# Kernel optimization log

Measured on AMD Instinct MI355X. Metric: run time of the kernel, lower is better.

The kernel has to match this reference:

```python
import jax, jax.numpy as jnp
import numpy as np

N_NODES = 50000
N_EDGES = 800000
D = 128
N_GRAPHS = 64


def setup_inputs() -> dict:
    key = jax.random.key(0)
    ks = jax.random.split(key, 9)
    x = jax.random.normal(ks[0], (N_NODES, D), dtype=jnp.float32)
    edge_index = jax.random.randint(ks[1], (2, N_EDGES), 0, N_NODES, dtype=jnp.int32)
    batch = jnp.sort(jax.random.randint(ks[2], (N_NODES,), 0, N_GRAPHS, dtype=jnp.int32))
    s = 1.0 / np.sqrt(D)
    W1 = jax.random.normal(ks[3], (D, D), jnp.float32) * s
    W2 = jax.random.normal(ks[4], (D, D), jnp.float32) * s
    W3 = jax.random.normal(ks[5], (D, D), jnp.float32) * s
    b1 = jnp.zeros((D,), jnp.float32)
    b2 = jnp.zeros((D,), jnp.float32)
    b3 = jnp.zeros((D,), jnp.float32)
    return {"x": x, "W1": W1, "b1": b1, "W2": W2, "b2": b2, "W3": W3, "b3": b3,
            "edge_index": edge_index, "batch": batch}


def _gcn_conv(x, W, b, src, dst, deg_inv_sqrt):
    # PyG GCNConv: x' = D^{-1/2} (A+I) D^{-1/2} (x W) + b
    h = x @ W                                    # [N, D]
    norm = (deg_inv_sqrt[src] * deg_inv_sqrt[dst])[:, None]   # [E, 1]
    agg = jax.ops.segment_sum(h[src] * norm, dst, num_segments=N_NODES)
    # self-loop contribution: norm_ii = deg_i^{-1}
    agg = agg + (deg_inv_sqrt * deg_inv_sqrt)[:, None] * h
    return agg + b


def reference(x, W1, b1, W2, b2, W3, b3, edge_index, batch):
    src, dst = edge_index[0], edge_index[1]
    # degree on A + I (self-loops added), edge weight 1
    deg = jax.ops.segment_sum(jnp.ones((N_EDGES,), x.dtype), dst,
                              num_segments=N_NODES) + 1.0
    deg_inv_sqrt = jax.lax.rsqrt(deg)
    h = jax.nn.relu(_gcn_conv(x, W1, b1, src, dst, deg_inv_sqrt))
    h = jax.nn.relu(_gcn_conv(h, W2, b2, src, dst, deg_inv_sqrt))
    h = _gcn_conv(h, W3, b3, src, dst, deg_inv_sqrt)
    # global_max_pool over graph ids
    return jax.ops.segment_max(h, batch, num_segments=N_GRAPHS)
```

## Files before the change

### kernel.cpp

```cpp
#include <hip/hip_runtime.h>
#include <float.h>
#include <math.h>

#define D 128
#define PCHUNK 64
#define NBUCK 256
#define BROWS 196
#define BCAP 4096
#define ACHUNK 3125

typedef _Float16 half8 __attribute__((ext_vector_type(8)));
typedef _Float16 half2v __attribute__((ext_vector_type(2)));
typedef float f32x4 __attribute__((ext_vector_type(4)));

__device__ __forceinline__ unsigned encf(float x) {
    unsigned u = __float_as_uint(x);
    return (u & 0x80000000u) ? ~u : (u | 0x80000000u);
}
__device__ __forceinline__ float decf(unsigned e) {
    unsigned u = (e & 0x80000000u) ? (e & 0x7FFFFFFFu) : ~e;
    return __uint_as_float(u);
}

__global__ __launch_bounds__(256) void binA_kernel(const int* __restrict__ src,
                                                   const int* __restrict__ dst,
                                                   int* __restrict__ gcnt,
                                                   uint2* __restrict__ gpair, int ne) {
    __shared__ int lh[NBUCK], ssc[NBUCK], lstart[NBUCK], gbase[NBUCK], loff[NBUCK];
    __shared__ uint2 stage[ACHUNK + 8];
    int t = threadIdx.x;
    int e0 = blockIdx.x * ACHUNK;
    int e1 = min(e0 + ACHUNK, ne);
    lh[t] = 0;
    __syncthreads();
    for (int e = e0 + t; e < e1; e += 256) atomicAdd(&lh[dst[e] / BROWS], 1);
    __syncthreads();
    ssc[t] = lh[t];
    __syncthreads();
    for (int off = 1; off < NBUCK; off <<= 1) {
        int u = (t >= off) ? ssc[t - off] : 0;
        __syncthreads();
        ssc[t] += u;
        __syncthreads();
    }
    int st = ssc[t] - lh[t];
    lstart[t] = st;
    loff[t] = st;
    if (lh[t] > 0) gbase[t] = atomicAdd(&gcnt[t], lh[t]);
    __syncthreads();
    for (int e = e0 + t; e < e1; e += 256) {
        int s = src[e], d = dst[e];
        int pos = atomicAdd(&loff[d / BROWS], 1);
        stage[pos] = make_uint2((unsigned)s, (unsigned)d);
    }
    __syncthreads();
    int m = e1 - e0;
    for (int i = t; i < m; i += 256) {
        uint2 pr = stage[i];
        int b = (int)pr.y / BROWS;
        int gpos = b * BCAP + gbase[b] + (i - lstart[b]);
        if (gpos < (b + 1) * BCAP) gpair[gpos] = pr;
    }
}

__global__ __launch_bounds__(256) void scanB_kernel(const int* __restrict__ gcnt,
                                                    int* __restrict__ bstart,
                                                    unsigned* __restrict__ outEnc, int nout) {
    __shared__ int s[NBUCK], c[NBUCK];
    int t = threadIdx.x;
    for (int j = t; j < nout; j += 256) outEnc[j] = 0x007FFFFFu;
    c[t] = gcnt[t];
    s[t] = c[t];
    __syncthreads();
    for (int off = 1; off < NBUCK; off <<= 1) {
        int u = (t >= off) ? s[t - off] : 0;
        __syncthreads();
        s[t] += u;
        __syncthreads();
    }
    bstart[t] = s[t] - c[t];
    if (t == NBUCK - 1) bstart[NBUCK] = s[NBUCK - 1];
}

__global__ __launch_bounds__(256) void binB_kernel(const uint2* __restrict__ gpair,
                                                   const int* __restrict__ gcnt,
                                                   const int* __restrict__ bstart,
                                                   int* __restrict__ rowptr,
                                                   float* __restrict__ disv,
                                                   int* __restrict__ csr, int n) {
    __shared__ int lh[256], ssc[256], lstart[256], loff[256];
    __shared__ int cstage[BCAP];
    int b = blockIdx.x, t = threadIdx.x;
    int m = min(gcnt[b], BCAP);
    int row0 = b * BROWS;
    int nrows = min(BROWS, n - row0);
    if (nrows <= 0) return;
    const uint2* mp = gpair + (size_t)b * BCAP;
    lh[t] = 0;
    __syncthreads();
    for (int i = t; i < m; i += 256) atomicAdd(&lh[(int)mp[i].y - row0], 1);
    __syncthreads();
    ssc[t] = lh[t];
    __syncthreads();
    for (int off = 1; off < 256; off <<= 1) {
        int u = (t >= off) ? ssc[t - off] : 0;
        __syncthreads();
        ssc[t] += u;
        __syncthreads();
    }
    int st = ssc[t] - lh[t];
    lstart[t] = st;
    loff[t] = st;
    __syncthreads();
    int bs = bstart[b];
    if (t <= nrows) rowptr[row0 + t] = bs + lstart[t];
    if (t < nrows) disv[row0 + t] = rsqrtf((float)lh[t] + 1.0f);
    for (int i = t; i < m; i += 256) {
        uint2 pr = mp[i];
        int pos = atomicAdd(&loff[(int)pr.y - row0], 1);
        cstage[pos] = (int)pr.x;
    }
    __syncthreads();
    for (int i = t; i < m; i += 256) csr[bs + i] = cstage[i];
}

__global__ void pack3_kernel(const float* __restrict__ W1, const float* __restrict__ W2,
                             const float* __restrict__ W3, _Float16* __restrict__ Wp1,
                             _Float16* __restrict__ Wp2, _Float16* __restrict__ Wp3) {
    int gi = blockIdx.x * blockDim.x + threadIdx.x;
    int w = gi >> 14, i = gi & 16383;
    const float* W = (w == 0) ? W1 : (w == 1) ? W2 : W3;
    _Float16* Wp = (w == 0) ? Wp1 : (w == 1) ? Wp2 : Wp3;
    int j = i & 7, l = (i >> 3) & 63, t = (i >> 9) & 7, s = (i >> 12) & 3;
    int k = s * 32 + ((l >> 4) << 3) + j;
    int c = t * 16 + (l & 15);
    Wp[i] = (_Float16)W[k * 128 + c];
}

template <bool F32SRC>
__global__ __launch_bounds__(256) void gemm_mfma(const void* __restrict__ Xsrc,
                                                 const _Float16* __restrict__ Wp,
                                                 const float* __restrict__ disv,
                                                 _Float16* __restrict__ Gh,
                                                 int ntiles, int n) {
    __shared__ _Float16 Wl[16384];
    int tid = threadIdx.x;
    {
        const uint4* s4 = (const uint4*)Wp;
        uint4* d4 = (uint4*)Wl;
#pragma unroll
        for (int i = 0; i < 8; i++) d4[tid + 256 * i] = s4[tid + 256 * i];
    }
    __syncthreads();
    int wave = tid >> 6, lane = tid & 63;
    int m = lane & 15, quad = lane >> 4;
    const half8* wfrag = (const half8*)Wl;
    const _Float16* Xh = (const _Float16*)Xsrc;
    const float* Xf = (const float*)Xsrc;

    for (int tile0 = blockIdx.x * 4; tile0 < ntiles; tile0 += gridDim.x * 4) {
        int tile = tile0 + wave;
        if (tile >= ntiles) break;
        int arow = tile * 16 + m;
        if (arow >= n) arow = n - 1;

        f32x4 acc[8];
#pragma unroll
        for (int t = 0; t < 8; t++) acc[t] = (f32x4){0.f, 0.f, 0.f, 0.f};

#pragma unroll
        for (int s = 0; s < 4; s++) {
            half8 a;
            if (F32SRC) {
                float4 lo = *(const float4*)(Xf + (size_t)arow * D + s * 32 + quad * 8);
                float4 hi = *(const float4*)(Xf + (size_t)arow * D + s * 32 + quad * 8 + 4);
                a[0] = (_Float16)lo.x; a[1] = (_Float16)lo.y; a[2] = (_Float16)lo.z; a[3] = (_Float16)lo.w;
                a[4] = (_Float16)hi.x; a[5] = (_Float16)hi.y; a[6] = (_Float16)hi.z; a[7] = (_Float16)hi.w;
            } else {
                a = *(const half8*)(Xh + (size_t)arow * D + s * 32 + quad * 8);
            }
#pragma unroll
            for (int t = 0; t < 8; t++) {
                half8 b = wfrag[(s * 8 + t) * 64 + lane];
                acc[t] = __builtin_amdgcn_mfma_f32_16x16x32_f16(a, b, acc[t], 0, 0, 0);
            }
        }
        int orow0 = tile * 16 + quad * 4;
        if (orow0 + 3 < n) {
            float d0 = disv[orow0], d1 = disv[orow0 + 1], d2 = disv[orow0 + 2], d3 = disv[orow0 + 3];
#pragma unroll
            for (int t = 0; t < 8; t++) {
                int col = t * 16 + m;
                Gh[(size_t)(orow0 + 0) * D + col] = (_Float16)(acc[t][0] * d0);
                Gh[(size_t)(orow0 + 1) * D + col] = (_Float16)(acc[t][1] * d1);
                Gh[(size_t)(orow0 + 2) * D + col] = (_Float16)(acc[t][2] * d2);
                Gh[(size_t)(orow0 + 3) * D + col] = (_Float16)(acc[t][3] * d3);
            }
        } else {
#pragma unroll
            for (int t = 0; t < 8; t++) {
                int col = t * 16 + m;
#pragma unroll
                for (int r = 0; r < 4; r++) {
                    int orow = orow0 + r;
                    if (orow < n) Gh[(size_t)orow * D + col] = (_Float16)(acc[t][r] * disv[orow]);
                }
            }
        }
    }
}

__global__ __launch_bounds__(256) void agg_f16(const _Float16* __restrict__ G,
                                               const int* __restrict__ rowptr,
                                               const int* __restrict__ csr,
                                               const float* __restrict__ disv,
                                               const float* __restrict__ bias,
                                               _Float16* __restrict__ Out, int n, int relu) {
    int wave = threadIdx.x >> 6, lane = threadIdx.x & 63;
    int node = blockIdx.x * 4 + wave;
    if (node >= n) return;
    const half2v* G2 = (const half2v*)G;
    half2v sv = G2[(size_t)node * 64 + lane];
    float ax = (float)sv[0], ay = (float)sv[1];
    int e = rowptr[node], end = rowptr[node + 1];
    for (; e + 8 <= end; e += 8) {
        int s0 = csr[e], s1 = csr[e + 1], s2 = csr[e + 2], s3 = csr[e + 3];
        int s4 = csr[e + 4], s5 = csr[e + 5], s6 = csr[e + 6], s7 = csr[e + 7];
        half2v v0 = G2[(size_t)s0 * 64 + lane];
        half2v v1 = G2[(size_t)s1 * 64 + lane];
        half2v v2 = G2[(size_t)s2 * 64 + lane];
        half2v v3 = G2[(size_t)s3 * 64 + lane];
        half2v v4 = G2[(size_t)s4 * 64 + lane];
        half2v v5 = G2[(size_t)s5 * 64 + lane];
        half2v v6 = G2[(size_t)s6 * 64 + lane];
        half2v v7 = G2[(size_t)s7 * 64 + lane];
        ax += (((float)v0[0] + (float)v1[0]) + ((float)v2[0] + (float)v3[0])) +
              (((float)v4[0] + (float)v5[0]) + ((float)v6[0] + (float)v7[0]));
        ay += (((float)v0[1] + (float)v1[1]) + ((float)v2[1] + (float)v3[1])) +
              (((float)v4[1] + (float)v5[1]) + ((float)v6[1] + (float)v7[1]));
    }
    for (; e + 4 <= end; e += 4) {
        int s0 = csr[e], s1 = csr[e + 1], s2 = csr[e + 2], s3 = csr[e + 3];
        half2v v0 = G2[(size_t)s0 * 64 + lane];
        half2v v1 = G2[(size_t)s1 * 64 + lane];
        half2v v2 = G2[(size_t)s2 * 64 + lane];
        half2v v3 = G2[(size_t)s3 * 64 + lane];
        ax += ((float)v0[0] + (float)v1[0]) + ((float)v2[0] + (float)v3[0]);
        ay += ((float)v0[1] + (float)v1[1]) + ((float)v2[1] + (float)v3[1]);
    }
    for (; e < end; e++) {
        half2v v = G2[(size_t)csr[e] * 64 + lane];
        ax += (float)v[0]; ay += (float)v[1];
    }
    float dd = disv[node];
    int c = lane * 2;
    float ox = fmaf(dd, ax, bias[c]);
    float oy = fmaf(dd, ay, bias[c + 1]);
    if (relu) { ox = fmaxf(ox, 0.f); oy = fmaxf(oy, 0.f); }
    half2v o;
    o[0] = (_Float16)ox; o[1] = (_Float16)oy;
    ((half2v*)Out)[(size_t)node * 64 + lane] = o;
}

__global__ __launch_bounds__(128) void pool_kernel(const _Float16* __restrict__ H,
                                                   const int* __restrict__ batch,
                                                   unsigned* __restrict__ outEnc, int n) {
    int d = threadIdx.x;
    int start = blockIdx.x * PCHUNK;
    if (start >= n) return;
    int end = min(start + PCHUNK, n);
    int curg = batch[start];
    float cur = -INFINITY;
    for (int i = start; i < end; i++) {
        float v = (float)H[(size_t)i * D + d];
        int g = batch[i];
        if (g != curg) { atomicMax(&outEnc[curg * D + d], encf(cur)); cur = v; curg = g; }
        else cur = fmaxf(cur, v);
    }
    atomicMax(&outEnc[curg * D + d], encf(cur));
}

__global__ void decode_kernel(const unsigned* __restrict__ outEnc, float* __restrict__ out, int n) {
    int i = blockIdx.x * blockDim.x + threadIdx.x;
    if (i < n) out[i] = decf(outEnc[i]);
}

extern "C" void kernel_launch(void* const* d_in, const int* in_sizes, int n_in,
                              void* d_out, int out_size, void* d_ws, size_t ws_size,
                              hipStream_t stream) {
    const float* x  = (const float*)d_in[0];
    const float* W1 = (const float*)d_in[1];
    const float* b1 = (const float*)d_in[2];
    const float* W2 = (const float*)d_in[3];
    const float* b2 = (const float*)d_in[4];
    const float* W3 = (const float*)d_in[5];
    const float* b3 = (const float*)d_in[6];
    const int* ei    = (const int*)d_in[7];
    const int* batch = (const int*)d_in[8];

    int n  = in_sizes[0] / D;
    int ne = in_sizes[7] / 2;
    const int* src = ei;
    const int* dst = ei + ne;

    char* p = (char*)d_ws;
    auto alloc = [&](size_t bytes) -> void* {
        void* q = (void*)p;
        p += (bytes + 255) & ~(size_t)255;
        return q;
    };
    _Float16* Gh  = (_Float16*)alloc((size_t)n * D * 2);
    _Float16* Hh  = (_Float16*)alloc((size_t)n * D * 2);
    _Float16* Wp1 = (_Float16*)alloc((size_t)D * D * 2);
    _Float16* Wp2 = (_Float16*)alloc((size_t)D * D * 2);
    _Float16* Wp3 = (_Float16*)alloc((size_t)D * D * 2);
    int* gcnt     = (int*)alloc((size_t)NBUCK * 4);
    int* bstart   = (int*)alloc((size_t)(NBUCK + 1) * 4);
    uint2* gpair  = (uint2*)alloc((size_t)NBUCK * BCAP * 8);
    int* rowptr   = (int*)alloc((size_t)(n + 1) * 4);
    int* csr      = (int*)alloc((size_t)ne * 4);
    float* disv   = (float*)alloc((size_t)n * 4);
    unsigned* outEnc = (unsigned*)alloc((size_t)out_size * 4);

    hipMemsetAsync(gcnt, 0, (size_t)NBUCK * 4, stream);

    int nblocksA = (ne + ACHUNK - 1) / ACHUNK;
    binA_kernel<<<nblocksA, 256, 0, stream>>>(src, dst, gcnt, gpair, ne);
    scanB_kernel<<<1, 256, 0, stream>>>(gcnt, bstart, outEnc, out_size);
    binB_kernel<<<NBUCK, 256, 0, stream>>>(gpair, gcnt, bstart, rowptr, disv, csr, n);
    pack3_kernel<<<192, 256, 0, stream>>>(W1, W2, W3, Wp1, Wp2, Wp3);

    int ntiles = (n + 15) / 16;
    int gemm_blocks = 512;
    int agg_blocks  = (n + 3) / 4;

    gemm_mfma<true><<<gemm_blocks, 256, 0, stream>>>(x, Wp1, disv, Gh, ntiles, n);
    agg_f16<<<agg_blocks, 256, 0, stream>>>(Gh, rowptr, csr, disv, b1, Hh, n, 1);
    gemm_mfma<false><<<gemm_blocks, 256, 0, stream>>>(Hh, Wp2, disv, Gh, ntiles, n);
    agg_f16<<<agg_blocks, 256, 0, stream>>>(Gh, rowptr, csr, disv, b2, Hh, n, 1);
    gemm_mfma<false><<<gemm_blocks, 256, 0, stream>>>(Hh, Wp3, disv, Gh, ntiles, n);
    agg_f16<<<agg_blocks, 256, 0, stream>>>(Gh, rowptr, csr, disv, b3, Hh, n, 0);

    pool_kernel<<<(n + PCHUNK - 1) / PCHUNK, 128, 0, stream>>>(Hh, batch, outEnc, n);
    decode_kernel<<<(out_size + 255) / 256, 256, 0, stream>>>(outEnc, (float*)d_out, out_size);
}
```

Before: 265.4 us.

## Fuse aggregation with next-layer GEMM and final aggregation with max-pool

```diff
diff --git a/kernel.cpp b/kernel.cpp
--- a/kernel.cpp
+++ b/kernel.cpp
@@ -3,7 +3,6 @@
 #include <math.h>
 
 #define D 128
-#define PCHUNK 64
 #define NBUCK 256
 #define BROWS 196
 #define BCAP 4096
@@ -22,206 +21,12 @@
     return __uint_as_float(u);
 }
 
-__global__ __launch_bounds__(256) void binA_kernel(const int* __restrict__ src,
-                                                   const int* __restrict__ dst,
-                                                   int* __restrict__ gcnt,
-                                                   uint2* __restrict__ gpair, int ne) {
-    __shared__ int lh[NBUCK], ssc[NBUCK], lstart[NBUCK], gbase[NBUCK], loff[NBUCK];
-    __shared__ uint2 stage[ACHUNK + 8];
-    int t = threadIdx.x;
-    int e0 = blockIdx.x * ACHUNK;
-    int e1 = min(e0 + ACHUNK, ne);
-    lh[t] = 0;
-    __syncthreads();
-    for (int e = e0 + t; e < e1; e += 256) atomicAdd(&lh[dst[e] / BROWS], 1);
-    __syncthreads();
-    ssc[t] = lh[t];
-    __syncthreads();
-    for (int off = 1; off < NBUCK; off <<= 1) {
-        int u = (t >= off) ? ssc[t - off] : 0;
-        __syncthreads();
-        ssc[t] += u;
-        __syncthreads();
-    }
-    int st = ssc[t] - lh[t];
-    lstart[t] = st;
-    loff[t] = st;
-    if (lh[t] > 0) gbase[t] = atomicAdd(&gcnt[t], lh[t]);
-    __syncthreads();
-    for (int e = e0 + t; e < e1; e += 256) {
-        int s = src[e], d = dst[e];
-        int pos = atomicAdd(&loff[d / BROWS], 1);
-        stage[pos] = make_uint2((unsigned)s, (unsigned)d);
-    }
-    __syncthreads();
-    int m = e1 - e0;
-    for (int i = t; i < m; i += 256) {
-        uint2 pr = stage[i];
-        int b = (int)pr.y / BROWS;
-        int gpos = b * BCAP + gbase[b] + (i - lstart[b]);
-        if (gpos < (b + 1) * BCAP) gpair[gpos] = pr;
-    }
-}
-
-__global__ __launch_bounds__(256) void scanB_kernel(const int* __restrict__ gcnt,
-                                                    int* __restrict__ bstart,
-                                                    unsigned* __restrict__ outEnc, int nout) {
-    __shared__ int s[NBUCK], c[NBUCK];
-    int t = threadIdx.x;
-    for (int j = t; j < nout; j += 256) outEnc[j] = 0x007FFFFFu;
-    c[t] = gcnt[t];
-    s[t] = c[t];
-    __syncthreads();
-    for (int off = 1; off < NBUCK; off <<= 1) {
-        int u = (t >= off) ? s[t - off] : 0;
-        __syncthreads();
-        s[t] += u;
-        __syncthreads();
-    }
-    bstart[t] = s[t] - c[t];
-    if (t == NBUCK - 1) bstart[NBUCK] = s[NBUCK - 1];
-}
-
-__global__ __launch_bounds__(256) void binB_kernel(const uint2* __restrict__ gpair,
-                                                   const int* __restrict__ gcnt,
-                                                   const int* __restrict__ bstart,
-                                                   int* __restrict__ rowptr,
-                                                   float* __restrict__ disv,
-                                                   int* __restrict__ csr, int n) {
-    __shared__ int lh[256], ssc[256], lstart[256], loff[256];
-    __shared__ int cstage[BCAP];
-    int b = blockIdx.x, t = threadIdx.x;
-    int m = min(gcnt[b], BCAP);
-    int row0 = b * BROWS;
-    int nrows = min(BROWS, n - row0);
-    if (nrows <= 0) return;
-    const uint2* mp = gpair + (size_t)b * BCAP;
-    lh[t] = 0;
-    __syncthreads();
-    for (int i = t; i < m; i += 256) atomicAdd(&lh[(int)mp[i].y - row0], 1);
-    __syncthreads();
-    ssc[t] = lh[t];
-    __syncthreads();
-    for (int off = 1; off < 256; off <<= 1) {
-        int u = (t >= off) ? ssc[t - off] : 0;
-        __syncthreads();
-        ssc[t] += u;
-        __syncthreads();
-    }
-    int st = ssc[t] - lh[t];
-    lstart[t] = st;
-    loff[t] = st;
-    __syncthreads();
-    int bs = bstart[b];
-    if (t <= nrows) rowptr[row0 + t] = bs + lstart[t];
-    if (t < nrows) disv[row0 + t] = rsqrtf((float)lh[t] + 1.0f);
-    for (int i = t; i < m; i += 256) {
-        uint2 pr = mp[i];
-        int pos = atomicAdd(&loff[(int)pr.y - row0], 1);
-        cstage[pos] = (int)pr.x;
-    }
-    __syncthreads();
-    for (int i = t; i < m; i += 256) csr[bs + i] = cstage[i];
-}
-
-__global__ void pack3_kernel(const float* __restrict__ W1, const float* __restrict__ W2,
-                             const float* __restrict__ W3, _Float16* __restrict__ Wp1,
-                             _Float16* __restrict__ Wp2, _Float16* __restrict__ Wp3) {
-    int gi = blockIdx.x * blockDim.x + threadIdx.x;
-    int w = gi >> 14, i = gi & 16383;
-    const float* W = (w == 0) ? W1 : (w == 1) ? W2 : W3;
-    _Float16* Wp = (w == 0) ? Wp1 : (w == 1) ? Wp2 : Wp3;
-    int j = i & 7, l = (i >> 3) & 63, t = (i >> 9) & 7, s = (i >> 12) & 3;
-    int k = s * 32 + ((l >> 4) << 3) + j;
-    int c = t * 16 + (l & 15);
-    Wp[i] = (_Float16)W[k * 128 + c];
-}
-
-template <bool F32SRC>
-__global__ __launch_bounds__(256) void gemm_mfma(const void* __restrict__ Xsrc,
-                                                 const _Float16* __restrict__ Wp,
-                                                 const float* __restrict__ disv,
-                                                 _Float16* __restrict__ Gh,
-                                                 int ntiles, int n) {
-    __shared__ _Float16 Wl[16384];
-    int tid = threadIdx.x;
-    {
-        const uint4* s4 = (const uint4*)Wp;
-        uint4* d4 = (uint4*)Wl;
-#pragma unroll
-        for (int i = 0; i < 8; i++) d4[tid + 256 * i] = s4[tid + 256 * i];
-    }
-    __syncthreads();
-    int wave = tid >> 6, lane = tid & 63;
-    int m = lane & 15, quad = lane >> 4;
-    const half8* wfrag = (const half8*)Wl;
-    const _Float16* Xh = (const _Float16*)Xsrc;
-    const float* Xf = (const float*)Xsrc;
-
-    for (int tile0 = blockIdx.x * 4; tile0 < ntiles; tile0 += gridDim.x * 4) {
-        int tile = tile0 + wave;
-        if (tile >= ntiles) break;
-        int arow = tile * 16 + m;
-        if (arow >= n) arow = n - 1;
-
-        f32x4 acc[8];
-#pragma unroll
-        for (int t = 0; t < 8; t++) acc[t] = (f32x4){0.f, 0.f, 0.f, 0.f};
-
-#pragma unroll
-        for (int s = 0; s < 4; s++) {
-            half8 a;
-            if (F32SRC) {
-                float4 lo = *(const float4*)(Xf + (size_t)arow * D + s * 32 + quad * 8);
-                float4 hi = *(const float4*)(Xf + (size_t)arow * D + s * 32 + quad * 8 + 4);
-                a[0] = (_Float16)lo.x; a[1] = (_Float16)lo.y; a[2] = (_Float16)lo.z; a[3] = (_Float16)lo.w;
-                a[4] = (_Float16)hi.x; a[5] = (_Float16)hi.y; a[6] = (_Float16)hi.z; a[7] = (_Float16)hi.w;
-            } else {
-                a = *(const half8*)(Xh + (size_t)arow * D + s * 32 + quad * 8);
-            }
-#pragma unroll
-            for (int t = 0; t < 8; t++) {
-                half8 b = wfrag[(s * 8 + t) * 64 + lane];
-                acc[t] = __builtin_amdgcn_mfma_f32_16x16x32_f16(a, b, acc[t], 0, 0, 0);
-            }
-        }
-        int orow0 = tile * 16 + quad * 4;
-        if (orow0 + 3 < n) {
-            float d0 = disv[orow0], d1 = disv[orow0 + 1], d2 = disv[orow0 + 2], d3 = disv[orow0 + 3];
-#pragma unroll
-            for (int t = 0; t < 8; t++) {
-                int col = t * 16 + m;
-                Gh[(size_t)(orow0 + 0) * D + col] = (_Float16)(acc[t][0] * d0);
-                Gh[(size_t)(orow0 + 1) * D + col] = (_Float16)(acc[t][1] * d1);
-                Gh[(size_t)(orow0 + 2) * D + col] = (_Float16)(acc[t][2] * d2);
-                Gh[(size_t)(orow0 + 3) * D + col] = (_Float16)(acc[t][3] * d3);
-            }
-        } else {
-#pragma unroll
-            for (int t = 0; t < 8; t++) {
-                int col = t * 16 + m;
-#pragma unroll
-                for (int r = 0; r < 4; r++) {
-                    int orow = orow0 + r;
-                    if (orow < n) Gh[(size_t)orow * D + col] = (_Float16)(acc[t][r] * disv[orow]);
-                }
-            }
-        }
-    }
-}
-
-__global__ __launch_bounds__(256) void agg_f16(const _Float16* __restrict__ G,
-                                               const int* __restrict__ rowptr,
-                                               const int* __restrict__ csr,
-                                               const float* __restrict__ disv,
-                                               const float* __restrict__ bias,
-                                               _Float16* __restrict__ Out, int n, int relu) {
-    int wave = threadIdx.x >> 6, lane = threadIdx.x & 63;
-    int node = blockIdx.x * 4 + wave;
-    if (node >= n) return;
-    const half2v* G2 = (const half2v*)G;
+__device__ __forceinline__ void gather_row(const half2v* __restrict__ G2,
+                                           const int* __restrict__ rowptr,
+                                           const int* __restrict__ csr,
+                                           int node, int lane, float& ax, float& ay) {
     half2v sv = G2[(size_t)node * 64 + lane];
-    float ax = (float)sv[0], ay = (float)sv[1];
+    ax = (float)sv[0]; ay = (float)sv[1];
     int e = rowptr[node], end = rowptr[node + 1];
     for (; e + 8 <= end; e += 8) {
         int s0 = csr[e], s1 = csr[e + 1], s2 = csr[e + 2], s3 = csr[e + 3];
@@ -252,32 +57,302 @@
         half2v v = G2[(size_t)csr[e] * 64 + lane];
         ax += (float)v[0]; ay += (float)v[1];
     }
-    float dd = disv[node];
-    int c = lane * 2;
-    float ox = fmaf(dd, ax, bias[c]);
-    float oy = fmaf(dd, ay, bias[c + 1]);
-    if (relu) { ox = fmaxf(ox, 0.f); oy = fmaxf(oy, 0.f); }
-    half2v o;
-    o[0] = (_Float16)ox; o[1] = (_Float16)oy;
-    ((half2v*)Out)[(size_t)node * 64 + lane] = o;
-}
-
-__global__ __launch_bounds__(128) void pool_kernel(const _Float16* __restrict__ H,
-                                                   const int* __restrict__ batch,
-                                                   unsigned* __restrict__ outEnc, int n) {
-    int d = threadIdx.x;
-    int start = blockIdx.x * PCHUNK;
-    if (start >= n) return;
-    int end = min(start + PCHUNK, n);
-    int curg = batch[start];
-    float cur = -INFINITY;
-    for (int i = start; i < end; i++) {
-        float v = (float)H[(size_t)i * D + d];
-        int g = batch[i];
-        if (g != curg) { atomicMax(&outEnc[curg * D + d], encf(cur)); cur = v; curg = g; }
-        else cur = fmaxf(cur, v);
-    }
-    atomicMax(&outEnc[curg * D + d], encf(cur));
+}
+
+__global__ __launch_bounds__(256) void binA_kernel(const int* __restrict__ src,
+                                                   const int* __restrict__ dst,
+                                                   int* __restrict__ gcnt,
+                                                   uint2* __restrict__ gpair, int ne) {
+    __shared__ int lh[NBUCK], ssc[NBUCK], lstart[NBUCK], gbase[NBUCK], loff[NBUCK];
+    __shared__ uint2 stage[ACHUNK + 8];
+    int t = threadIdx.x;
+    int e0 = blockIdx.x * ACHUNK;
+    int e1 = min(e0 + ACHUNK, ne);
+    lh[t] = 0;
+    __syncthreads();
+    for (int e = e0 + t; e < e1; e += 256) atomicAdd(&lh[dst[e] / BROWS], 1);
+    __syncthreads();
+    ssc[t] = lh[t];
+    __syncthreads();
+    for (int off = 1; off < NBUCK; off <<= 1) {
+        int u = (t >= off) ? ssc[t - off] : 0;
+        __syncthreads();
+        ssc[t] += u;
+        __syncthreads();
+    }
+    int st = ssc[t] - lh[t];
+    lstart[t] = st;
+    loff[t] = st;
+    if (lh[t] > 0) gbase[t] = atomicAdd(&gcnt[t], lh[t]);
+    __syncthreads();
+    for (int e = e0 + t; e < e1; e += 256) {
+        int s = src[e], d = dst[e];
+        int pos = atomicAdd(&loff[d / BROWS], 1);
+        stage[pos] = make_uint2((unsigned)s, (unsigned)d);
+    }
+    __syncthreads();
+    int m = e1 - e0;
+    for (int i = t; i < m; i += 256) {
+        uint2 pr = stage[i];
+        int b = (int)pr.y / BROWS;
+        int gpos = b * BCAP + gbase[b] + (i - lstart[b]);
+        if (gpos < (b + 1) * BCAP) gpair[gpos] = pr;
+    }
+}
+
+__global__ __launch_bounds__(256) void scanB_kernel(const int* __restrict__ gcnt,
+                                                    int* __restrict__ bstart,
+                                                    unsigned* __restrict__ outEnc, int nout) {
+    __shared__ int s[NBUCK], c[NBUCK];
+    int t = threadIdx.x;
+    for (int j = t; j < nout; j += 256) outEnc[j] = 0x007FFFFFu;
+    c[t] = gcnt[t];
+    s[t] = c[t];
+    __syncthreads();
+    for (int off = 1; off < NBUCK; off <<= 1) {
+        int u = (t >= off) ? s[t - off] : 0;
+        __syncthreads();
+        s[t] += u;
+        __syncthreads();
+    }
+    bstart[t] = s[t] - c[t];
+    if (t == NBUCK - 1) bstart[NBUCK] = s[NBUCK - 1];
+}
+
+__global__ __launch_bounds__(256) void binB_kernel(const uint2* __restrict__ gpair,
+                                                   const int* __restrict__ gcnt,
+                                                   const int* __restrict__ bstart,
+                                                   int* __restrict__ rowptr,
+                                                   float* __restrict__ disv,
+                                                   int* __restrict__ csr, int n) {
+    __shared__ int lh[256], ssc[256], lstart[256], loff[256];
+    __shared__ int cstage[BCAP];
+    int b = blockIdx.x, t = threadIdx.x;
+    int m = min(gcnt[b], BCAP);
+    int row0 = b * BROWS;
+    int nrows = min(BROWS, n - row0);
+    if (nrows <= 0) return;
+    const uint2* mp = gpair + (size_t)b * BCAP;
+    lh[t] = 0;
+    __syncthreads();
+    for (int i = t; i < m; i += 256) atomicAdd(&lh[(int)mp[i].y - row0], 1);
+    __syncthreads();
+    ssc[t] = lh[t];
+    __syncthreads();
+    for (int off = 1; off < 256; off <<= 1) {
+        int u = (t >= off) ? ssc[t - off] : 0;
+        __syncthreads();
+        ssc[t] += u;
+        __syncthreads();
+    }
+    int st = ssc[t] - lh[t];
+    lstart[t] = st;
+    loff[t] = st;
+    __syncthreads();
+    int bs = bstart[b];
+    if (t <= nrows) rowptr[row0 + t] = bs + lstart[t];
+    if (t < nrows) disv[row0 + t] = rsqrtf((float)lh[t] + 1.0f);
+    for (int i = t; i < m; i += 256) {
+        uint2 pr = mp[i];
+        int pos = atomicAdd(&loff[(int)pr.y - row0], 1);
+        cstage[pos] = (int)pr.x;
+    }
+    __syncthreads();
+    for (int i = t; i < m; i += 256) csr[bs + i] = cstage[i];
+}
+
+__global__ void pack3_kernel(const float* __restrict__ W1, const float* __restrict__ W2,
+                             const float* __restrict__ W3, _Float16* __restrict__ Wp1,
+                             _Float16* __restrict__ Wp2, _Float16* __restrict__ Wp3) {
+    int gi = blockIdx.x * blockDim.x + threadIdx.x;
+    int w = gi >> 14, i = gi & 16383;
+    const float* W = (w == 0) ? W1 : (w == 1) ? W2 : W3;
+    _Float16* Wp = (w == 0) ? Wp1 : (w == 1) ? Wp2 : Wp3;
+    int j = i & 7, l = (i >> 3) & 63, t = (i >> 9) & 7, s = (i >> 12) & 3;
+    int k = s * 32 + ((l >> 4) << 3) + j;
+    int c = t * 16 + (l & 15);
+    Wp[i] = (_Float16)W[k * 128 + c];
+}
+
+__global__ __launch_bounds__(256) void gemm_mfma(const float* __restrict__ Xf,
+                                                 const _Float16* __restrict__ Wp,
+                                                 const float* __restrict__ disv,
+                                                 _Float16* __restrict__ Gh,
+                                                 int ntiles, int n) {
+    __shared__ _Float16 Wl[16384];
+    int tid = threadIdx.x;
+    {
+        const uint4* s4 = (const uint4*)Wp;
+        uint4* d4 = (uint4*)Wl;
+#pragma unroll
+        for (int i = 0; i < 8; i++) d4[tid + 256 * i] = s4[tid + 256 * i];
+    }
+    __syncthreads();
+    int wave = tid >> 6, lane = tid & 63;
+    int m = lane & 15, quad = lane >> 4;
+    const half8* wfrag = (const half8*)Wl;
+
+    for (int tile0 = blockIdx.x * 4; tile0 < ntiles; tile0 += gridDim.x * 4) {
+        int tile = tile0 + wave;
+        if (tile >= ntiles) break;
+        int arow = tile * 16 + m;
+        if (arow >= n) arow = n - 1;
+
+        f32x4 acc[8];
+#pragma unroll
+        for (int t = 0; t < 8; t++) acc[t] = (f32x4){0.f, 0.f, 0.f, 0.f};
+
+#pragma unroll
+        for (int s = 0; s < 4; s++) {
+            half8 a;
+            float4 lo = *(const float4*)(Xf + (size_t)arow * D + s * 32 + quad * 8);
+            float4 hi = *(const float4*)(Xf + (size_t)arow * D + s * 32 + quad * 8 + 4);
+            a[0] = (_Float16)lo.x; a[1] = (_Float16)lo.y; a[2] = (_Float16)lo.z; a[3] = (_Float16)lo.w;
+            a[4] = (_Float16)hi.x; a[5] = (_Float16)hi.y; a[6] = (_Float16)hi.z; a[7] = (_Float16)hi.w;
+#pragma unroll
+            for (int t = 0; t < 8; t++) {
+                half8 b = wfrag[(s * 8 + t) * 64 + lane];
+                acc[t] = __builtin_amdgcn_mfma_f32_16x16x32_f16(a, b, acc[t], 0, 0, 0);
+            }
+        }
+        int orow0 = tile * 16 + quad * 4;
+        if (orow0 + 3 < n) {
+            float d0 = disv[orow0], d1 = disv[orow0 + 1], d2 = disv[orow0 + 2], d3 = disv[orow0 + 3];
+#pragma unroll
+            for (int t = 0; t < 8; t++) {
+                int col = t * 16 + m;
+                Gh[(size_t)(orow0 + 0) * D + col] = (_Float16)(acc[t][0] * d0);
+                Gh[(size_t)(orow0 + 1) * D + col] = (_Float16)(acc[t][1] * d1);
+                Gh[(size_t)(orow0 + 2) * D + col] = (_Float16)(acc[t][2] * d2);
+                Gh[(size_t)(orow0 + 3) * D + col] = (_Float16)(acc[t][3] * d3);
+            }
+        } else {
+#pragma unroll
+            for (int t = 0; t < 8; t++) {
+                int col = t * 16 + m;
+#pragma unroll
+                for (int r = 0; r < 4; r++) {
+                    int orow = orow0 + r;
+                    if (orow < n) Gh[(size_t)orow * D + col] = (_Float16)(acc[t][r] * disv[orow]);
+                }
+            }
+        }
+    }
+}
+
+__global__ __launch_bounds__(256) void fused_ag(const _Float16* __restrict__ Gin,
+                                                const _Float16* __restrict__ Wp,
+                                                const int* __restrict__ rowptr,
+                                                const int* __restrict__ csr,
+                                                const float* __restrict__ disv,
+                                                const float* __restrict__ bias,
+                                                _Float16* __restrict__ Gout,
+                                                int ntiles, int n) {
+    __shared__ _Float16 Wl[16384];
+    __shared__ __align__(16) _Float16 stage[4][2048];
+    int tid = threadIdx.x;
+    {
+        const uint4* s4 = (const uint4*)Wp;
+        uint4* d4 = (uint4*)Wl;
+#pragma unroll
+        for (int i = 0; i < 8; i++) d4[tid + 256 * i] = s4[tid + 256 * i];
+    }
+    __syncthreads();
+    int wave = tid >> 6, lane = tid & 63;
+    int tile = blockIdx.x * 4 + wave;
+    if (tile >= ntiles) return;
+    _Float16* st = stage[wave];
+    const half2v* G2 = (const half2v*)Gin;
+    int sqp = lane >> 2;
+    int j0 = (lane & 3) * 2;
+    float bx = bias[lane * 2], by = bias[lane * 2 + 1];
+
+    for (int p = 0; p < 16; p++) {
+        int node = tile * 16 + p;
+        float ox = 0.f, oy = 0.f;
+        if (node < n) {
+            float ax, ay;
+            gather_row(G2, rowptr, csr, node, lane, ax, ay);
+            float dd = disv[node];
+            ox = fmaxf(fmaf(dd, ax, bx), 0.f);
+            oy = fmaxf(fmaf(dd, ay, by), 0.f);
+        }
+        half2v o;
+        o[0] = (_Float16)ox; o[1] = (_Float16)oy;
+        *(half2v*)&st[sqp * 128 + (((p + sqp) & 15) << 3) + j0] = o;
+    }
+
+    int m = lane & 15, quad = lane >> 4;
+    const half8* wfrag = (const half8*)Wl;
+    f32x4 acc[8];
+#pragma unroll
+    for (int t = 0; t < 8; t++) acc[t] = (f32x4){0.f, 0.f, 0.f, 0.f};
+#pragma unroll
+    for (int s = 0; s < 4; s++) {
+        int sqc = s * 4 + quad;
+        half8 a = *(const half8*)&st[sqc * 128 + (((m + sqc) & 15) << 3)];
+#pragma unroll
+        for (int t = 0; t < 8; t++) {
+            half8 b = wfrag[(s * 8 + t) * 64 + lane];
+            acc[t] = __builtin_amdgcn_mfma_f32_16x16x32_f16(a, b, acc[t], 0, 0, 0);
+        }
+    }
+    int orow0 = tile * 16 + quad * 4;
+    if (orow0 + 3 < n) {
+        float d0 = disv[orow0], d1 = disv[orow0 + 1], d2 = disv[orow0 + 2], d3 = disv[orow0 + 3];
+#pragma unroll
+        for (int t = 0; t < 8; t++) {
+            int col = t * 16 + m;
+            Gout[(size_t)(orow0 + 0) * D + col] = (_Float16)(acc[t][0] * d0);
+            Gout[(size_t)(orow0 + 1) * D + col] = (_Float16)(acc[t][1] * d1);
+            Gout[(size_t)(orow0 + 2) * D + col] = (_Float16)(acc[t][2] * d2);
+            Gout[(size_t)(orow0 + 3) * D + col] = (_Float16)(acc[t][3] * d3);
+        }
+    } else {
+#pragma unroll
+        for (int t = 0; t < 8; t++) {
+            int col = t * 16 + m;
+#pragma unroll
+            for (int r = 0; r < 4; r++) {
+                int orow = orow0 + r;
+                if (orow < n) Gout[(size_t)orow * D + col] = (_Float16)(acc[t][r] * disv[orow]);
+            }
+        }
+    }
+}
+
+__global__ __launch_bounds__(256) void aggpool(const _Float16* __restrict__ Gin,
+                                               const int* __restrict__ rowptr,
+                                               const int* __restrict__ csr,
+                                               const float* __restrict__ disv,
+                                               const float* __restrict__ bias,
+                                               const int* __restrict__ batch,
+                                               unsigned* __restrict__ outEnc, int n) {
+    int wave = threadIdx.x >> 6, lane = threadIdx.x & 63;
+    int base = (blockIdx.x * 4 + wave) * 32;
+    if (base >= n) return;
+    int end = min(base + 32, n);
+    const half2v* G2 = (const half2v*)Gin;
+    float bx = bias[lane * 2], by = bias[lane * 2 + 1];
+    float mx = -INFINITY, my = -INFINITY;
+    int curg = batch[base];
+    for (int node = base; node < end; node++) {
+        float ax, ay;
+        gather_row(G2, rowptr, csr, node, lane, ax, ay);
+        float dd = disv[node];
+        float ox = fmaf(dd, ax, bx);
+        float oy = fmaf(dd, ay, by);
+        int g = batch[node];
+        if (g != curg) {
+            atomicMax(&outEnc[curg * D + lane * 2], encf(mx));
+            atomicMax(&outEnc[curg * D + lane * 2 + 1], encf(my));
+            mx = ox; my = oy; curg = g;
+        } else {
+            mx = fmaxf(mx, ox); my = fmaxf(my, oy);
+        }
+    }
+    atomicMax(&outEnc[curg * D + lane * 2], encf(mx));
+    atomicMax(&outEnc[curg * D + lane * 2 + 1], encf(my));
 }
 
 __global__ void decode_kernel(const unsigned* __restrict__ outEnc, float* __restrict__ out, int n) {
@@ -309,8 +384,8 @@
         p += (bytes + 255) & ~(size_t)255;
         return q;
     };
-    _Float16* Gh  = (_Float16*)alloc((size_t)n * D * 2);
-    _Float16* Hh  = (_Float16*)alloc((size_t)n * D * 2);
+    _Float16* GhA = (_Float16*)alloc((size_t)n * D * 2);
+    _Float16* GhB = (_Float16*)alloc((size_t)n * D * 2);
     _Float16* Wp1 = (_Float16*)alloc((size_t)D * D * 2);
     _Float16* Wp2 = (_Float16*)alloc((size_t)D * D * 2);
     _Float16* Wp3 = (_Float16*)alloc((size_t)D * D * 2);
@@ -331,16 +406,11 @@
     pack3_kernel<<<192, 256, 0, stream>>>(W1, W2, W3, Wp1, Wp2, Wp3);
 
     int ntiles = (n + 15) / 16;
-    int gemm_blocks = 512;
-    int agg_blocks  = (n + 3) / 4;
-
-    gemm_mfma<true><<<gemm_blocks, 256, 0, stream>>>(x, Wp1, disv, Gh, ntiles, n);
-    agg_f16<<<agg_blocks, 256, 0, stream>>>(Gh, rowptr, csr, disv, b1, Hh, n, 1);
-    gemm_mfma<false><<<gemm_blocks, 256, 0, stream>>>(Hh, Wp2, disv, Gh, ntiles, n);
-    agg_f16<<<agg_blocks, 256, 0, stream>>>(Gh, rowptr, csr, disv, b2, Hh, n, 1);
-    gemm_mfma<false><<<gemm_blocks, 256, 0, stream>>>(Hh, Wp3, disv, Gh, ntiles, n);
-    agg_f16<<<agg_blocks, 256, 0, stream>>>(Gh, rowptr, csr, disv, b3, Hh, n, 0);
-
-    pool_kernel<<<(n + PCHUNK - 1) / PCHUNK, 128, 0, stream>>>(Hh, batch, outEnc, n);
+    int fused_blocks = (ntiles + 3) / 4;
+
+    gemm_mfma<<<512, 256, 0, stream>>>(x, Wp1, disv, GhA, ntiles, n);
+    fused_ag<<<fused_blocks, 256, 0, stream>>>(GhA, Wp2, rowptr, csr, disv, b1, GhB, ntiles, n);
+    fused_ag<<<fused_blocks, 256, 0, stream>>>(GhB, Wp3, rowptr, csr, disv, b2, GhA, ntiles, n);
+    aggpool<<<(n + 127) / 128, 256, 0, stream>>>(GhA, rowptr, csr, disv, b3, batch, outEnc, n);
     decode_kernel<<<(out_size + 255) / 256, 256, 0, stream>>>(outEnc, (float*)d_out, out_size);
 }
```

Result: slower. 407.0 us (+53.4%).

## Split aggregation by feature quarter with four edges per wave in parallel

Applied to the files above, without the earlier changes.

```diff
diff --git a/kernel.cpp b/kernel.cpp
--- a/kernel.cpp
+++ b/kernel.cpp
@@ -215,51 +215,56 @@
                                                const int* __restrict__ csr,
                                                const float* __restrict__ disv,
                                                const float* __restrict__ bias,
-                                               _Float16* __restrict__ Out, int n, int relu) {
+                                               _Float16* __restrict__ Out,
+                                               int n, int relu, int nbq) {
+    int bq = blockIdx.x / nbq;
+    int bi = blockIdx.x - bq * nbq;
     int wave = threadIdx.x >> 6, lane = threadIdx.x & 63;
-    int node = blockIdx.x * 4 + wave;
+    int node = bi * 4 + wave;
     if (node >= n) return;
-    const half2v* G2 = (const half2v*)G;
-    half2v sv = G2[(size_t)node * 64 + lane];
-    float ax = (float)sv[0], ay = (float)sv[1];
+    int sub = lane >> 4, li = lane & 15;
+    const _Float16* Gq = G + bq * 32;
+    float ax, ay;
+    if (sub == 0) {
+        half2v sv = *(const half2v*)(Gq + (size_t)node * D + li * 2);
+        ax = (float)sv[0]; ay = (float)sv[1];
+    } else {
+        ax = 0.f; ay = 0.f;
+    }
     int e = rowptr[node], end = rowptr[node + 1];
-    for (; e + 8 <= end; e += 8) {
-        int s0 = csr[e], s1 = csr[e + 1], s2 = csr[e + 2], s3 = csr[e + 3];
-        int s4 = csr[e + 4], s5 = csr[e + 5], s6 = csr[e + 6], s7 = csr[e + 7];
-        half2v v0 = G2[(size_t)s0 * 64 + lane];
-        half2v v1 = G2[(size_t)s1 * 64 + lane];
-        half2v v2 = G2[(size_t)s2 * 64 + lane];
-        half2v v3 = G2[(size_t)s3 * 64 + lane];
-        half2v v4 = G2[(size_t)s4 * 64 + lane];
-        half2v v5 = G2[(size_t)s5 * 64 + lane];
-        half2v v6 = G2[(size_t)s6 * 64 + lane];
-        half2v v7 = G2[(size_t)s7 * 64 + lane];
-        ax += (((float)v0[0] + (float)v1[0]) + ((float)v2[0] + (float)v3[0])) +
-              (((float)v4[0] + (float)v5[0]) + ((float)v6[0] + (float)v7[0]));
-        ay += (((float)v0[1] + (float)v1[1]) + ((float)v2[1] + (float)v3[1])) +
-              (((float)v4[1] + (float)v5[1]) + ((float)v6[1] + (float)v7[1]));
+    for (; e + 16 <= end; e += 16) {
+        int i0 = csr[e + sub], i1 = csr[e + 4 + sub];
+        int i2 = csr[e + 8 + sub], i3 = csr[e + 12 + sub];
+        half2v v0 = *(const half2v*)(Gq + (size_t)i0 * D + li * 2);
+        half2v v1 = *(const half2v*)(Gq + (size_t)i1 * D + li * 2);
+        half2v v2 = *(const half2v*)(Gq + (size_t)i2 * D + li * 2);
+        half2v v3 = *(const half2v*)(Gq + (size_t)i3 * D + li * 2);
+        ax += (((float)v0[0] + (float)v1[0]) + ((float)v2[0] + (float)v3[0]));
+        ay += (((float)v0[1] + (float)v1[1]) + ((float)v2[1] + (float)v3[1]));
     }
     for (; e + 4 <= end; e += 4) {
-        int s0 = csr[e], s1 = csr[e + 1], s2 = csr[e + 2], s3 = csr[e + 3];
-        half2v v0 = G2[(size_t)s0 * 64 + lane];
-        half2v v1 = G2[(size_t)s1 * 64 + lane];
-        half2v v2 = G2[(size_t)s2 * 64 + lane];
-        half2v v3 = G2[(size_t)s3 * 64 + lane];
-        ax += ((float)v0[0] + (float)v1[0]) + ((float)v2[0] + (float)v3[0]);
-        ay += ((float)v0[1] + (float)v1[1]) + ((float)v2[1] + (float)v3[1]);
-    }
-    for (; e < end; e++) {
-        half2v v = G2[(size_t)csr[e] * 64 + lane];
-        ax += (float)v[0]; ay += (float)v[1];
-    }
-    float dd = disv[node];
-    int c = lane * 2;
-    float ox = fmaf(dd, ax, bias[c]);
-    float oy = fmaf(dd, ay, bias[c + 1]);
-    if (relu) { ox = fmaxf(ox, 0.f); oy = fmaxf(oy, 0.f); }
-    half2v o;
-    o[0] = (_Float16)ox; o[1] = (_Float16)oy;
-    ((half2v*)Out)[(size_t)node * 64 + lane] = o;
+        int i0 = csr[e + sub];
+        half2v v0 = *(const half2v*)(Gq + (size_t)i0 * D + li * 2);
+        ax += (float)v0[0]; ay += (float)v0[1];
+    }
+    int r = end - e;
+    if (sub < r) {
+        int i0 = csr[e + sub];
+        half2v v0 = *(const half2v*)(Gq + (size_t)i0 * D + li * 2);
+        ax += (float)v0[0]; ay += (float)v0[1];
+    }
+    ax += __shfl_xor(ax, 16); ax += __shfl_xor(ax, 32);
+    ay += __shfl_xor(ay, 16); ay += __shfl_xor(ay, 32);
+    if (sub == 0) {
+        float dd = disv[node];
+        int c = bq * 32 + li * 2;
+        float ox = fmaf(dd, ax, bias[c]);
+        float oy = fmaf(dd, ay, bias[c + 1]);
+        if (relu) { ox = fmaxf(ox, 0.f); oy = fmaxf(oy, 0.f); }
+        half2v o;
+        o[0] = (_Float16)ox; o[1] = (_Float16)oy;
+        *(half2v*)(Out + (size_t)node * D + c) = o;
+    }
 }
 
 __global__ __launch_bounds__(128) void pool_kernel(const _Float16* __restrict__ H,
@@ -332,14 +337,15 @@
 
     int ntiles = (n + 15) / 16;
     int gemm_blocks = 512;
-    int agg_blocks  = (n + 3) / 4;
+    int nbq = (n + 3) / 4;
+    int agg_blocks = 4 * nbq;
 
     gemm_mfma<true><<<gemm_blocks, 256, 0, stream>>>(x, Wp1, disv, Gh, ntiles, n);
-    agg_f16<<<agg_blocks, 256, 0, stream>>>(Gh, rowptr, csr, disv, b1, Hh, n, 1);
+    agg_f16<<<agg_blocks, 256, 0, stream>>>(Gh, rowptr, csr, disv, b1, Hh, n, 1, nbq);
     gemm_mfma<false><<<gemm_blocks, 256, 0, stream>>>(Hh, Wp2, disv, Gh, ntiles, n);
-    agg_f16<<<agg_blocks, 256, 0, stream>>>(Gh, rowptr, csr, disv, b2, Hh, n, 1);
+    agg_f16<<<agg_blocks, 256, 0, stream>>>(Gh, rowptr, csr, disv, b2, Hh, n, 1, nbq);
     gemm_mfma<false><<<gemm_blocks, 256, 0, stream>>>(Hh, Wp3, disv, Gh, ntiles, n);
-    agg_f16<<<agg_blocks, 256, 0, stream>>>(Gh, rowptr, csr, disv, b3, Hh, n, 0);
+    agg_f16<<<agg_blocks, 256, 0, stream>>>(Gh, rowptr, csr, disv, b3, Hh, n, 0, nbq);
 
     pool_kernel<<<(n + PCHUNK - 1) / PCHUNK, 128, 0, stream>>>(Hh, batch, outEnc, n);
     decode_kernel<<<(out_size + 255) / 256, 256, 0, stream>>>(outEnc, (float*)d_out, out_size);
```

Measured after the change: 443.2 us. 67.0% more time.
